# Kernel optimization log

Measured on AMD Instinct MI355X. Metric: run time of the kernel, lower is better.

## Reference

```python
import jax, jax.numpy as jnp
import numpy as np

N_MEMORY, N_LOOPS, N_LATENT = 1067, 8, 128
N_CONTEXT = 64
MAX_FEAT = N_LOOPS * N_CONTEXT * N_LATENT  # 65536
BLOCK = 2048


def setup_inputs() -> dict:
    key = jax.random.key(0)
    ks = jax.random.split(key, 10)
    return {
        "memory": jax.random.normal(ks[0], (N_MEMORY, N_LOOPS, N_LATENT), jnp.float32),
        "z_in": jax.random.normal(ks[1], (N_LATENT,), jnp.float32),
        # scale weights so the F=65536 matvec output stays O(1)
        "weights": jax.random.normal(ks[2], (N_LOOPS, MAX_FEAT, N_LATENT), jnp.float32) * 0.005,
        "center": jax.random.normal(ks[3], (N_LOOPS, MAX_FEAT), jnp.float32),
        "bias": jax.random.normal(ks[4], (N_LOOPS, N_LATENT), jnp.float32),
        "z_min": jax.random.normal(ks[5], (N_LOOPS, N_LATENT), jnp.float32) - 2.0,
        "z_max": jax.random.normal(ks[6], (N_LOOPS, N_LATENT), jnp.float32) + 2.0,
        "limit_margin": jax.random.uniform(ks[7], (N_LATENT,), jnp.float32),
        "mask": jax.random.uniform(ks[8], (2, N_LOOPS), jnp.float32),
        "y_audio": jax.random.normal(ks[9], (N_LOOPS, 1, BLOCK), jnp.float32),
        "record_index": 500,
        "active_loop": 3,       # 1-indexed, as in LivingLooper.forward
        "latency_correct": 2,
        "context": N_CONTEXT,
    }


def _target_process_inv(z):
    # torch.where(z>1, 2*z**0.5 - 1, where(z<-1, 1 - 2*(-z)**0.5, z)); safe sqrt for jax where
    hi = 2.0 * jnp.sqrt(jnp.maximum(z, 1.0)) - 1.0
    lo = 1.0 - 2.0 * jnp.sqrt(jnp.maximum(-z, 1.0))
    return jnp.where(z > 1.0, hi, jnp.where(z < -1.0, lo, z))


def reference(memory, z_in, weights, center, bias, z_min, z_max,
              limit_margin, mask, y_audio, record_index, active_loop,
              latency_correct, context):
    n_memory, n_loops, n_latent = memory.shape
    i_act = active_loop - 1

    # --- ring-buffer record of new latent for active loop at dt = lc..0 ---
    rows = (record_index - np.arange(latency_correct + 1)) % n_memory
    mem1 = memory.at[rows, i_act].set(z_in)

    # --- get_frames(context, skip=1): context frames ending at record_index-1 ---
    widx = (record_index - 1 - context + 1 + np.arange(context)) % n_memory
    window = mem1[widx]                       # [ctx, n_loops, n_latent]
    flat = window.reshape(-1)                 # [F], F = ctx*n_loops*n_latent

    # --- per-loop Loop.eval: feat_process -> matvec -> inv -> clamp ---
    x = jnp.tanh((flat[None, :] - center) * 0.5)          # [L, F]
    z = jnp.einsum('lf,lfd->ld', x, weights) + bias       # [L, D]
    z = _target_process_inv(z)
    z = jnp.clip(z, z_min - limit_margin[None, :], z_max + limit_margin[None, :])

    # --- scatter eval results at record_index for all loops except active ---
    keep = (jnp.arange(n_loops) == i_act)[:, None]
    mem2 = mem1.at[record_index].set(jnp.where(keep, mem1[record_index], z))

    zs = mem2[record_index]                   # [L, D] == get_frames(1)

    # --- masked crossfade on decoded audio ---
    fade = jnp.linspace(0.0, 1.0, y_audio.shape[2])
    m = mask[1][:, None, None] * fade + mask[0][:, None, None] * (1.0 - fade)
    y = y_audio * m                           # [L, 1, block]
    return (y, zs, mem2)
```

## Files before the change

kernel.cpp:

```cpp
#include <hip/hip_runtime.h>

typedef float v4f __attribute__((ext_vector_type(4)));


__global__ __launch_bounds__(256) void ll_main_kernel(
    const float* __restrict__ memory, const float* __restrict__ z_in,
    const float* __restrict__ weights, const float* __restrict__ center,
    const float* __restrict__ mask, const float* __restrict__ y_audio,
    const int* __restrict__ rec_p, const int* __restrict__ act_p,
    const int* __restrict__ lc_p, const int* __restrict__ ctx_p,
    float* __restrict__ partials, float* __restrict__ out_y,
    float* __restrict__ out_mem2,
    int L, int F, int n_memory, int blocksPerLoop, int BLK,
    int Dsh, int LDsh, int BLKsh)
{
    __shared__ float x_lds[256];
    __shared__ float ps[8 * 128];

    const int D  = 1 << Dsh;
    const int LD = 1 << LDsh;

    const int bid = blockIdx.x;
    const int l = bid / blocksPerLoop;
    const int chunk = bid - l * blocksPerLoop;
    const int f0 = chunk * 256;
    const int tid = threadIdx.x;
    const int w = tid >> 6;
    const int p = (tid >> 5) & 1;
    const int t = tid & 31;
    const int rbase = (w << 6) + p;

    const int rec = *rec_p;
    const int i_act = *act_p - 1;
    const int lc = *lc_p;
    const int ctx = *ctx_p;

    const v4f* __restrict__ Wv =
        (const v4f*)(weights + ((size_t)(l * F + f0) << Dsh)) + (rbase << 5) + t;

    v4f pre[8];
    #pragma unroll
    for (int j = 0; j < 8; ++j) pre[j] = Wv[j << 6];

    {
        const int f = f0 + tid;
        const int c = f >> LDsh;
        const int rem = f & (LD - 1);
        const int ll = rem >> Dsh;
        const int dd = rem & (D - 1);
        int row = rec - ctx + c;
        if (row < 0) row += n_memory;
        const int dt = ctx - c;
        const float v = (ll == i_act && dt <= lc)
                            ? z_in[dd]
                            : memory[((size_t)row << LDsh) + rem];
        const float cen = center[(size_t)l * F + f];
        x_lds[tid] = tanhf((v - cen) * 0.5f);
    }
    __syncthreads();

    v4f acc = (v4f)0.f;
    #pragma unroll
    for (int j = 0; j < 8; ++j) acc += x_lds[rbase + (j << 1)] * pre[j];
    #pragma unroll 8
    for (int i = 8; i < 32; ++i)
        acc += x_lds[rbase + (i << 1)] * Wv[i << 6];

    ((v4f*)&ps[(tid >> 5) << 7])[t] = acc;
    __syncthreads();

    if (tid < 128) {
        float s = 0.f;
        #pragma unroll
        for (int gg = 0; gg < 8; ++gg) s += ps[(gg << 7) + tid];
        partials[((size_t)bid << 7) + tid] = s;
    }

    const int gsize = gridDim.x * 256;
    const int Ncopy4 = (n_memory << LDsh) >> 2;
    const int total4 = Ncopy4 + ((L * BLK) >> 2);
    for (int i4 = bid * 256 + tid; i4 < total4; i4 += gsize) {
        if (i4 < Ncopy4) {
            const int idx = i4 << 2;
            const int row = idx >> LDsh;
            if (row == rec) continue;
            const int rem = idx & (LD - 1);
            const int ll = rem >> Dsh;
            const int dd = rem & (D - 1);
            int diff = rec - row; if (diff < 0) diff += n_memory;
            v4f v;
            if (ll == i_act && diff <= lc) v = *(const v4f*)(z_in + dd);
            else                           v = *(const v4f*)(memory + idx);
            __builtin_nontemporal_store(v, (v4f*)(out_mem2 + idx));
        } else {
            const int j = (i4 - Ncopy4) << 2;
            const int li = j >> BLKsh;
            const int k = j & ((1 << BLKsh) - 1);
            const float inv = 1.f / (float)((1 << BLKsh) - 1);
            const float m0 = mask[li], m1 = mask[L + li];
            const v4f ya = *(const v4f*)(y_audio + j);
            v4f r;
            #pragma unroll
            for (int e = 0; e < 4; ++e) {
                const float fade = (float)(k + e) * inv;
                r[e] = ya[e] * (m1 * fade + m0 * (1.f - fade));
            }
            *(v4f*)(out_y + j) = r;
        }
    }
}

__global__ __launch_bounds__(256) void ll_finalize_kernel(
    const float* __restrict__ partials, const float* __restrict__ bias,
    const float* __restrict__ z_min, const float* __restrict__ z_max,
    const float* __restrict__ limit_margin, const float* __restrict__ z_in,
    const int* __restrict__ rec_p, const int* __restrict__ act_p,
    float* __restrict__ out_zs, float* __restrict__ out_mem2,
    int L, int D, int blocksPerLoop)
{
    const int tid = blockIdx.x * blockDim.x + threadIdx.x;
    if (tid >= L * D) return;
    const int l = tid / D;
    const int d = tid - l * D;

    float s = 0.f;
    const float* __restrict__ p = partials + ((size_t)l * blocksPerLoop) * D + d;
    #pragma unroll 16
    for (int c = 0; c < blocksPerLoop; ++c)
        s += p[(size_t)c * D];

    float z = s + bias[tid];
    const float hi = 2.f * sqrtf(fmaxf(z, 1.f)) - 1.f;
    const float lo = 1.f - 2.f * sqrtf(fmaxf(-z, 1.f));
    z = (z > 1.f) ? hi : ((z < -1.f) ? lo : z);
    const float zl = z_min[tid] - limit_margin[d];
    const float zh = z_max[tid] + limit_margin[d];
    z = fminf(fmaxf(z, zl), zh);

    const float out = (l == (*act_p - 1)) ? z_in[d] : z;
    out_zs[tid] = out;
    out_mem2[(size_t)(*rec_p) * (L * D) + tid] = out;
}

extern "C" void kernel_launch(void* const* d_in, const int* in_sizes, int n_in,
                              void* d_out, int out_size, void* d_ws, size_t ws_size,
                              hipStream_t stream) {
    const float* memory       = (const float*)d_in[0];
    const float* z_in         = (const float*)d_in[1];
    const float* weights      = (const float*)d_in[2];
    const float* center       = (const float*)d_in[3];
    const float* bias         = (const float*)d_in[4];
    const float* z_min        = (const float*)d_in[5];
    const float* z_max        = (const float*)d_in[6];
    const float* limit_margin = (const float*)d_in[7];
    const float* mask         = (const float*)d_in[8];
    const float* y_audio      = (const float*)d_in[9];
    const int*   rec_p        = (const int*)d_in[10];
    const int*   act_p        = (const int*)d_in[11];
    const int*   lc_p         = (const int*)d_in[12];
    const int*   ctx_p        = (const int*)d_in[13];

    const int D        = in_sizes[1];
    const int L        = in_sizes[4] / D;
    const int LD       = L * D;
    const int n_memory = in_sizes[0] / LD;
    const int F        = in_sizes[3] / L;
    const int BLK      = in_sizes[9] / L;

    const int Dsh   = __builtin_ctz(D);
    const int LDsh  = __builtin_ctz(LD);
    const int BLKsh = __builtin_ctz(BLK);

    float* out_y    = (float*)d_out;
    float* out_zs   = out_y + (size_t)L * BLK;
    float* out_mem2 = out_zs + LD;

    float* partials = (float*)d_ws;

    const int blocksPerLoop = F / 256;
    ll_main_kernel<<<L * blocksPerLoop, 256, 0, stream>>>(
        memory, z_in, weights, center, mask, y_audio,
        rec_p, act_p, lc_p, ctx_p,
        partials, out_y, out_mem2,
        L, F, n_memory, blocksPerLoop, BLK, Dsh, LDsh, BLKsh);

    ll_finalize_kernel<<<(LD + 255) / 256, 256, 0, stream>>>(
        partials, bias, z_min, z_max, limit_margin, z_in,
        rec_p, act_p, out_zs, out_mem2, L, D, blocksPerLoop);
}
```

Measured before the change: 54.66 us.

## Dedicate separate blocks to memory copy and crossfade, widen matvec blocks to 512 threads

```diff
diff --git a/kernel.cpp b/kernel.cpp
--- a/kernel.cpp
+++ b/kernel.cpp
@@ -2,8 +2,10 @@
 
 typedef float v4f __attribute__((ext_vector_type(4)));
 
+#define NMISC 32
 
-__global__ __launch_bounds__(256) void ll_main_kernel(
+
+__global__ __launch_bounds__(512) void ll_main_kernel(
     const float* __restrict__ memory, const float* __restrict__ z_in,
     const float* __restrict__ weights, const float* __restrict__ center,
     const float* __restrict__ mask, const float* __restrict__ y_audio,
@@ -11,29 +13,66 @@
     const int* __restrict__ lc_p, const int* __restrict__ ctx_p,
     float* __restrict__ partials, float* __restrict__ out_y,
     float* __restrict__ out_mem2,
-    int L, int F, int n_memory, int blocksPerLoop, int BLK,
-    int Dsh, int LDsh, int BLKsh)
+    int L, int F, int n_memory, int BLK,
+    int Dsh, int LDsh, int BLKsh, int bplSh)
 {
-    __shared__ float x_lds[256];
-    __shared__ float ps[8 * 128];
-
     const int D  = 1 << Dsh;
     const int LD = 1 << LDsh;
-
     const int bid = blockIdx.x;
-    const int l = bid / blocksPerLoop;
-    const int chunk = bid - l * blocksPerLoop;
-    const int f0 = chunk * 256;
     const int tid = threadIdx.x;
-    const int w = tid >> 6;
-    const int p = (tid >> 5) & 1;
-    const int t = tid & 31;
-    const int rbase = (w << 6) + p;
 
     const int rec = *rec_p;
     const int i_act = *act_p - 1;
     const int lc = *lc_p;
-    const int ctx = *ctx_p;
+
+    if (bid < NMISC) {
+        const int gsize = NMISC * 512;
+        const int Ncopy4 = (n_memory << LDsh) >> 2;
+        const int total4 = Ncopy4 + ((L * BLK) >> 2);
+        for (int i4 = bid * 512 + tid; i4 < total4; i4 += gsize) {
+            if (i4 < Ncopy4) {
+                const int idx = i4 << 2;
+                const int row = idx >> LDsh;
+                if (row == rec) continue;
+                const int rem = idx & (LD - 1);
+                const int ll = rem >> Dsh;
+                const int dd = rem & (D - 1);
+                int diff = rec - row; if (diff < 0) diff += n_memory;
+                v4f v;
+                if (ll == i_act && diff <= lc) v = *(const v4f*)(z_in + dd);
+                else                           v = *(const v4f*)(memory + idx);
+                __builtin_nontemporal_store(v, (v4f*)(out_mem2 + idx));
+            } else {
+                const int j = (i4 - Ncopy4) << 2;
+                const int li = j >> BLKsh;
+                const int k = j & ((1 << BLKsh) - 1);
+                const float inv = 1.f / (float)((1 << BLKsh) - 1);
+                const float m0 = mask[li], m1 = mask[L + li];
+                const v4f ya = *(const v4f*)(y_audio + j);
+                v4f r;
+                #pragma unroll
+                for (int e = 0; e < 4; ++e) {
+                    const float fade = (float)(k + e) * inv;
+                    r[e] = ya[e] * (m1 * fade + m0 * (1.f - fade));
+                }
+                *(v4f*)(out_y + j) = r;
+            }
+        }
+        return;
+    }
+
+    __shared__ float x_lds[512];
+    __shared__ float ps[16 * 128];
+
+    const int mb = bid - NMISC;
+    const int l = mb >> bplSh;
+    const int chunk = mb & ((1 << bplSh) - 1);
+    const int f0 = chunk << 9;
+
+    const int w = tid >> 6;
+    const int par = (tid >> 5) & 1;
+    const int t = tid & 31;
+    const int rbase = (w << 6) + par;
 
     const v4f* __restrict__ Wv =
         (const v4f*)(weights + ((size_t)(l * F + f0) << Dsh)) + (rbase << 5) + t;
@@ -48,9 +87,9 @@
         const int rem = f & (LD - 1);
         const int ll = rem >> Dsh;
         const int dd = rem & (D - 1);
-        int row = rec - ctx + c;
+        int row = rec - (*ctx_p) + c;
         if (row < 0) row += n_memory;
-        const int dt = ctx - c;
+        const int dt = (*ctx_p) - c;
         const float v = (ll == i_act && dt <= lc)
                             ? z_in[dd]
                             : memory[((size_t)row << LDsh) + rem];
@@ -72,41 +111,8 @@
     if (tid < 128) {
         float s = 0.f;
         #pragma unroll
-        for (int gg = 0; gg < 8; ++gg) s += ps[(gg << 7) + tid];
-        partials[((size_t)bid << 7) + tid] = s;
-    }
-
-    const int gsize = gridDim.x * 256;
-    const int Ncopy4 = (n_memory << LDsh) >> 2;
-    const int total4 = Ncopy4 + ((L * BLK) >> 2);
-    for (int i4 = bid * 256 + tid; i4 < total4; i4 += gsize) {
-        if (i4 < Ncopy4) {
-            const int idx = i4 << 2;
-            const int row = idx >> LDsh;
-            if (row == rec) continue;
-            const int rem = idx & (LD - 1);
-            const int ll = rem >> Dsh;
-            const int dd = rem & (D - 1);
-            int diff = rec - row; if (diff < 0) diff += n_memory;
-            v4f v;
-            if (ll == i_act && diff <= lc) v = *(const v4f*)(z_in + dd);
-            else                           v = *(const v4f*)(memory + idx);
-            __builtin_nontemporal_store(v, (v4f*)(out_mem2 + idx));
-        } else {
-            const int j = (i4 - Ncopy4) << 2;
-            const int li = j >> BLKsh;
-            const int k = j & ((1 << BLKsh) - 1);
-            const float inv = 1.f / (float)((1 << BLKsh) - 1);
-            const float m0 = mask[li], m1 = mask[L + li];
-            const v4f ya = *(const v4f*)(y_audio + j);
-            v4f r;
-            #pragma unroll
-            for (int e = 0; e < 4; ++e) {
-                const float fade = (float)(k + e) * inv;
-                r[e] = ya[e] * (m1 * fade + m0 * (1.f - fade));
-            }
-            *(v4f*)(out_y + j) = r;
-        }
+        for (int gg = 0; gg < 16; ++gg) s += ps[(gg << 7) + tid];
+        partials[((size_t)mb << 7) + tid] = s;
     }
 }
 
@@ -116,7 +122,7 @@
     const float* __restrict__ limit_margin, const float* __restrict__ z_in,
     const int* __restrict__ rec_p, const int* __restrict__ act_p,
     float* __restrict__ out_zs, float* __restrict__ out_mem2,
-    int L, int D, int blocksPerLoop)
+    int L, int D, int bpl)
 {
     const int tid = blockIdx.x * blockDim.x + threadIdx.x;
     if (tid >= L * D) return;
@@ -124,9 +130,9 @@
     const int d = tid - l * D;
 
     float s = 0.f;
-    const float* __restrict__ p = partials + ((size_t)l * blocksPerLoop) * D + d;
+    const float* __restrict__ p = partials + ((size_t)l * bpl) * D + d;
     #pragma unroll 16
-    for (int c = 0; c < blocksPerLoop; ++c)
+    for (int c = 0; c < bpl; ++c)
         s += p[(size_t)c * D];
 
     float z = s + bias[tid];
@@ -170,6 +176,8 @@
     const int Dsh   = __builtin_ctz(D);
     const int LDsh  = __builtin_ctz(LD);
     const int BLKsh = __builtin_ctz(BLK);
+    const int bpl   = F >> 9;
+    const int bplSh = __builtin_ctz(bpl);
 
     float* out_y    = (float*)d_out;
     float* out_zs   = out_y + (size_t)L * BLK;
@@ -177,14 +185,14 @@
 
     float* partials = (float*)d_ws;
 
-    const int blocksPerLoop = F / 256;
-    ll_main_kernel<<<L * blocksPerLoop, 256, 0, stream>>>(
+    const int grid = NMISC + L * bpl;
+    ll_main_kernel<<<grid, 512, 0, stream>>>(
         memory, z_in, weights, center, mask, y_audio,
         rec_p, act_p, lc_p, ctx_p,
         partials, out_y, out_mem2,
-        L, F, n_memory, blocksPerLoop, BLK, Dsh, LDsh, BLKsh);
+        L, F, n_memory, BLK, Dsh, LDsh, BLKsh, bplSh);
 
     ll_finalize_kernel<<<(LD + 255) / 256, 256, 0, stream>>>(
         partials, bias, z_min, z_max, limit_margin, z_in,
-        rec_p, act_p, out_zs, out_mem2, L, D, blocksPerLoop);
+        rec_p, act_p, out_zs, out_mem2, L, D, bpl);
 }
```

New measurement: 53.15 us. 2.8% less time.
